# Kernel optimization log

Measured on AMD Instinct MI355X. Metric: run time of the kernel, lower is better.

## Reference

```python
import jax, jax.numpy as jnp
import numpy as np

K = 10        # neighbors
SIGMA = 1.0   # gaussian bandwidth
BIG = 1e9     # diagonal fill so a point is never its own neighbor


def _knn_idx(h, k):
    # h: (B, T, H) -> idx: (B, T, k) of nearest neighbors (euclidean), excluding self
    # squared-distance trick avoids materializing (B, T, T, H)
    sq = jnp.sum(h * h, axis=-1)                                  # (B, T)
    d2 = sq[:, :, None] + sq[:, None, :] - 2.0 * jnp.einsum('bth,bsh->bts', h, h)
    d = jnp.sqrt(jnp.maximum(d2, 0.0))                            # (B, T, T)
    T = h.shape[1]
    eye = jnp.eye(T, dtype=bool)
    d = jnp.where(eye[None, :, :], BIG, d)
    k_eff = min(k, T - 1)
    _, idx = jax.lax.top_k(-d, k_eff)                             # smallest distances
    return idx


def setup_inputs() -> dict:
    key = jax.random.key(0)
    ks = jax.random.split(key, 5)
    B, T, C, H = 64, 1024, 64, 32
    x = jax.random.normal(ks[0], (B, T, C), dtype=jnp.float32)
    s1 = 1.0 / np.sqrt(C)
    s2 = 1.0 / np.sqrt(H)
    W1 = jax.random.uniform(ks[1], (C, H), minval=-s1, maxval=s1, dtype=jnp.float32)
    b1 = jax.random.uniform(ks[2], (H,), minval=-s1, maxval=s1, dtype=jnp.float32)
    W2 = jax.random.uniform(ks[3], (H, H), minval=-s2, maxval=s2, dtype=jnp.float32)
    b2 = jax.random.uniform(ks[4], (H,), minval=-s2, maxval=s2, dtype=jnp.float32)
    return {"x": x, "W1": W1, "b1": b1, "W2": W2, "b2": b2}


def reference(x, W1, b1, W2, b2):
    h = x @ W1 + b1                                               # (B, T, H)
    # kNN graph built under no_grad in the original
    idx = _knn_idx(jax.lax.stop_gradient(h), K)                   # (B, T, k)
    # gather neighbors without the (B, T, T, H) expansion
    neigh = jax.vmap(lambda hb, ib: hb[ib])(h, idx)               # (B, T, k, H)
    diff = neigh - h[:, :, None, :]
    dist = jnp.sqrt(jnp.sum(diff * diff, axis=-1))                # (B, T, k)
    w = jnp.exp(-dist ** 2 / (2.0 * SIGMA ** 2 + 1e-8))
    w = w / (jnp.sum(w, axis=-1, keepdims=True) + 1e-8)
    smooth = jnp.einsum('btk,btkh->bth', w, neigh)                # (B, T, H)
    lap = h - smooth
    return jnp.tanh(lap) @ W2 + b2
```

## Files before the change

### kernel.cpp

```cpp
#include <hip/hip_runtime.h>
#include <math.h>

#define BB 64
#define TT 1024
#define CC 64
#define HH 32
#define KNN 10

typedef float v4f __attribute__((ext_vector_type(4)));
typedef _Float16 f16x8 __attribute__((ext_vector_type(8)));

__device__ __forceinline__ unsigned umn(unsigned a, unsigned b) { return a < b ? a : b; }
__device__ __forceinline__ unsigned umx(unsigned a, unsigned b) { return a > b ? a : b; }

__global__ __launch_bounds__(256) void h_kernel(
    const float* __restrict__ x, const float* __restrict__ W1,
    const float* __restrict__ b1, float* __restrict__ h, float* __restrict__ hsq)
{
    __shared__ float w1s[CC][HH];
    __shared__ float b1s[HH];
    int tid = threadIdx.x;
    for (int i = tid; i < CC * HH; i += 256) w1s[i >> 5][i & 31] = W1[i];
    if (tid < HH) b1s[tid] = b1[tid];
    __syncthreads();

    int row = blockIdx.x * 256 + tid;
    const float4* xr = (const float4*)(x + (size_t)row * CC);
    float acc[HH];
    #pragma unroll
    for (int j = 0; j < HH; ++j) acc[j] = b1s[j];
    #pragma unroll
    for (int c4 = 0; c4 < CC / 4; ++c4) {
        float4 xv = xr[c4];
        #pragma unroll
        for (int j = 0; j < HH; ++j) {
            acc[j] = fmaf(xv.x, w1s[c4 * 4 + 0][j], acc[j]);
            acc[j] = fmaf(xv.y, w1s[c4 * 4 + 1][j], acc[j]);
            acc[j] = fmaf(xv.z, w1s[c4 * 4 + 2][j], acc[j]);
            acc[j] = fmaf(xv.w, w1s[c4 * 4 + 3][j], acc[j]);
        }
    }
    float s = 0.f;
    #pragma unroll
    for (int j = 0; j < HH; ++j) s = fmaf(acc[j], acc[j], s);
    float* hr = h + (size_t)row * HH;
    #pragma unroll
    for (int q = 0; q < HH / 4; ++q) {
        float4 v = { acc[4*q], acc[4*q+1], acc[4*q+2], acc[4*q+3] };
        ((float4*)hr)[q] = v;
    }
    hsq[row] = 0.5f * s * 1048576.0f;
}

#define INSERT_PAIR(kE, kO) do {                                       \
    unsigned lo_ = umn(kE, kO), hi_ = umx(kE, kO);                     \
    bd9 = umn(umn(bd9, umx(bd8, lo_)), umx(bd7, hi_));                 \
    bd8 = umn(umn(bd8, umx(bd7, lo_)), umx(bd6, hi_));                 \
    bd7 = umn(umn(bd7, umx(bd6, lo_)), umx(bd5, hi_));                 \
    bd6 = umn(umn(bd6, umx(bd5, lo_)), umx(bd4, hi_));                 \
    bd5 = umn(umn(bd5, umx(bd4, lo_)), umx(bd3, hi_));                 \
    bd4 = umn(umn(bd4, umx(bd3, lo_)), umx(bd2, hi_));                 \
    bd3 = umn(umn(bd3, umx(bd2, lo_)), umx(bd1, hi_));                 \
    bd2 = umn(umn(bd2, umx(bd1, lo_)), umx(bd0, hi_));                 \
    bd1 = umn(umn(bd1, umx(bd0, lo_)), hi_);                           \
    bd0 = umn(bd0, lo_);                                               \
} while (0)

__global__ __launch_bounds__(512, 2) void lap_kernel(
    const float* __restrict__ h, const float* __restrict__ hsq,
    const float* __restrict__ W2, const float* __restrict__ b2,
    float* __restrict__ out)
{
    __shared__ _Float16 cah[2][2][64][40];
    __shared__ _Float16 cal[2][2][64][40];
    __shared__ unsigned s_key[8][64][KNN];
    __shared__ float e_wk[64][KNN];
    __shared__ short e_id[64][KNN];
    __shared__ float e_inv[64];
    __shared__ float w2s[HH][HH];
    __shared__ float b2s[HH];

    int tid  = threadIdx.x;
    int lane = tid & 63;
    int wid  = __builtin_amdgcn_readfirstlane(tid >> 6);

    int g   = blockIdx.x;
    int l   = g >> 3;
    int bb  = ((g & 7) << 3) | (l & 7);
    int rb  = (l >> 3) << 6;

    for (int i = tid; i < HH * HH; i += 512) w2s[i >> 5][i & 31] = W2[i];
    if (tid < HH) b2s[tid] = b2[tid];

    const float* hb  = h   + (size_t)bb * TT * HH;
    const float* sqb = hsq + (size_t)bb * TT;

    int gtg  = wid & 3;
    int half = wid >> 2;
    int n    = lane & 15;
    int kc   = lane >> 4;

    int trow = rb + gtg * 16 + n;
    f16x8 Bhi, Blo;
    {
        const float* tp = hb + (size_t)trow * HH + kc * 8;
        float4 f1 = ((const float4*)tp)[0];
        float4 f2 = ((const float4*)tp)[1];
        float tf[8] = { f1.x, f1.y, f1.z, f1.w, f2.x, f2.y, f2.z, f2.w };
        #pragma unroll
        for (int e = 0; e < 8; ++e) {
            _Float16 hh = (_Float16)tf[e];
            Bhi[e] = hh;
            Blo[e] = (_Float16)(tf[e] - (float)hh);
        }
    }
    float cinit20 = sqb[trow] + 1048576.0f;

    int s_local = trow - half * 512;
    bool selfok = ((unsigned)s_local < 512u) && (((s_local >> 2) & 3) == kc);
    int self_t7 = selfok ? (((s_local >> 6) << 4) | (((s_local >> 4) & 3) << 2)
                           | (s_local & 3)) : -1;

    unsigned bd0 = 0xFFFFFFFFu, bd1 = 0xFFFFFFFFu, bd2 = 0xFFFFFFFFu,
             bd3 = 0xFFFFFFFFu, bd4 = 0xFFFFFFFFu, bd5 = 0xFFFFFFFFu,
             bd6 = 0xFFFFFFFFu, bd7 = 0xFFFFFFFFu, bd8 = 0xFFFFFFFFu,
             bd9 = 0xFFFFFFFFu;

    int st_c = tid & 3, st_r = (tid >> 2) & 63, st_h = tid >> 8;

    auto STAGE = [&](int buf, int t) {
        const float* p = hb + (size_t)(st_h * 512 + t * 64 + st_r) * HH + st_c * 8;
        float4 f1 = ((const float4*)p)[0];
        float4 f2 = ((const float4*)p)[1];
        float fe[8] = { f1.x, f1.y, f1.z, f1.w, f2.x, f2.y, f2.z, f2.w };
        f16x8 hi8, lo8;
        #pragma unroll
        for (int e = 0; e < 8; ++e) {
            _Float16 hh = (_Float16)fe[e];
            hi8[e] = hh;
            lo8[e] = (_Float16)(fe[e] - (float)hh);
        }
        *(f16x8*)&cah[buf][st_h][st_r][st_c * 8] = hi8;
        *(f16x8*)&cal[buf][st_h][st_r][st_c * 8] = lo8;
    };

    STAGE(0, 0);
    __syncthreads();

    for (int t = 0; t < 8; ++t) {
        if (t < 7) STAGE((t + 1) & 1, t + 1);
        int buf = t & 1;
        #pragma unroll
        for (int sub = 0; sub < 4; ++sub) {
            f16x8 Ahi = *(const f16x8*)&cah[buf][half][sub * 16 + n][kc * 8];
            f16x8 Alo = *(const f16x8*)&cal[buf][half][sub * 16 + n][kc * 8];
            v4f acc = { 0.f, 0.f, 0.f, 0.f };
            acc = __builtin_amdgcn_mfma_f32_16x16x32_f16(Ahi, Bhi, acc, 0, 0, 0);
            acc = __builtin_amdgcn_mfma_f32_16x16x32_f16(Ahi, Blo, acc, 0, 0, 0);
            acc = __builtin_amdgcn_mfma_f32_16x16x32_f16(Alo, Bhi, acc, 0, 0, 0);
            const float4 hv = *(const float4*)(sqb + half * 512 + t * 64
                                               + sub * 16 + kc * 4);
            int t7b = (t << 4) | (sub << 2);
            float k0f = fmaf(acc[0], -1048576.0f, cinit20 + hv.x);
            float k1f = fmaf(acc[1], -1048576.0f, cinit20 + hv.y);
            float k2f = fmaf(acc[2], -1048576.0f, cinit20 + hv.z);
            float k3f = fmaf(acc[3], -1048576.0f, cinit20 + hv.w);
            unsigned p0 = (umn((unsigned)k0f, 0x1FFFFFFu) << 7) | (unsigned)(t7b + 0);
            unsigned p1 = (umn((unsigned)k1f, 0x1FFFFFFu) << 7) | (unsigned)(t7b + 1);
            unsigned p2 = (umn((unsigned)k2f, 0x1FFFFFFu) << 7) | (unsigned)(t7b + 2);
            unsigned p3 = (umn((unsigned)k3f, 0x1FFFFFFu) << 7) | (unsigned)(t7b + 3);
            p0 = (t7b + 0 == self_t7) ? 0xFFFFFFFFu : p0;
            p1 = (t7b + 1 == self_t7) ? 0xFFFFFFFFu : p1;
            p2 = (t7b + 2 == self_t7) ? 0xFFFFFFFFu : p2;
            p3 = (t7b + 3 == self_t7) ? 0xFFFFFFFFu : p3;
            INSERT_PAIR(p0, p1);
            INSERT_PAIR(p2, p3);
        }
        __syncthreads();
    }

    {
        int p  = half * 4 + kc;
        int tr = gtg * 16 + n;
        s_key[p][tr][0] = bd0; s_key[p][tr][1] = bd1;
        s_key[p][tr][2] = bd2; s_key[p][tr][3] = bd3;
        s_key[p][tr][4] = bd4; s_key[p][tr][5] = bd5;
        s_key[p][tr][6] = bd6; s_key[p][tr][7] = bd7;
        s_key[p][tr][8] = bd8; s_key[p][tr][9] = bd9;
    }
    __syncthreads();

    if (wid == 0) {
        unsigned k0 = s_key[0][lane][0], k1 = s_key[1][lane][0];
        unsigned k2 = s_key[2][lane][0], k3 = s_key[3][lane][0];
        unsigned k4 = s_key[4][lane][0], k5 = s_key[5][lane][0];
        unsigned k6 = s_key[6][lane][0], k7 = s_key[7][lane][0];
        int q0=0,q1=0,q2=0,q3=0,q4=0,q5=0,q6=0,q7=0;
        float wsum = 0.f;
        #pragma unroll
        for (int j = 0; j < KNN; ++j) {
            unsigned mn = k0; int c = 0;
            if (k1 < mn) { mn = k1; c = 1; }
            if (k2 < mn) { mn = k2; c = 2; }
            if (k3 < mn) { mn = k3; c = 3; }
            if (k4 < mn) { mn = k4; c = 4; }
            if (k5 < mn) { mn = k5; c = 5; }
            if (k6 < mn) { mn = k6; c = 6; }
            if (k7 < mn) { mn = k7; c = 7; }
            int t7 = (int)(mn & 127u);
            int abs_ = ((c >> 2) << 9) + ((t7 >> 4) << 6) + (((t7 >> 2) & 3) << 4)
                       + ((c & 3) << 2) + (t7 & 3);
            float kf = (float)(mn >> 7) * 9.5367431640625e-07f;
            float wk = expf(1.0f - kf);
            wsum += wk;
            e_id[lane][j] = (short)abs_;
            e_wk[lane][j] = wk;
            if      (c == 0) { ++q0; k0 = (q0 < KNN) ? s_key[0][lane][q0] : 0xFFFFFFFFu; }
            else if (c == 1) { ++q1; k1 = (q1 < KNN) ? s_key[1][lane][q1] : 0xFFFFFFFFu; }
            else if (c == 2) { ++q2; k2 = (q2 < KNN) ? s_key[2][lane][q2] : 0xFFFFFFFFu; }
            else if (c == 3) { ++q3; k3 = (q3 < KNN) ? s_key[3][lane][q3] : 0xFFFFFFFFu; }
            else if (c == 4) { ++q4; k4 = (q4 < KNN) ? s_key[4][lane][q4] : 0xFFFFFFFFu; }
            else if (c == 5) { ++q5; k5 = (q5 < KNN) ? s_key[5][lane][q5] : 0xFFFFFFFFu; }
            else if (c == 6) { ++q6; k6 = (q6 < KNN) ? s_key[6][lane][q6] : 0xFFFFFFFFu; }
            else             { ++q7; k7 = (q7 < KNN) ? s_key[7][lane][q7] : 0xFFFFFFFFu; }
        }
        e_inv[lane] = 1.0f / (wsum + 1e-8f);
    }
    __syncthreads();

    float* a_pool = (float*)&s_key[0][0][0];
    {
        int r  = tid >> 3;
        int g2 = (tid & 7) << 2;
        float ax = 0.f, ay = 0.f, az = 0.f, aw = 0.f;
        #pragma unroll
        for (int k = 0; k < KNN; ++k) {
            int idx  = e_id[r][k];
            float wk = e_wk[r][k];
            const float4 nv = *(const float4*)(hb + (size_t)idx * HH + g2);
            ax = fmaf(wk, nv.x, ax);
            ay = fmaf(wk, nv.y, ay);
            az = fmaf(wk, nv.z, az);
            aw = fmaf(wk, nv.w, aw);
        }
        float inv = e_inv[r];
        const float4 hv = *(const float4*)(hb + (size_t)(rb + r) * HH + g2);
        float4 av;
        av.x = tanhf(fmaf(-ax, inv, hv.x));
        av.y = tanhf(fmaf(-ay, inv, hv.y));
        av.z = tanhf(fmaf(-az, inv, hv.z));
        av.w = tanhf(fmaf(-aw, inv, hv.w));
        *(float4*)&a_pool[r * 36 + g2] = av;
    }
    __syncthreads();

    int r   = tid >> 3;
    int c0_ = (tid & 7) << 2;
    float o[4];
    #pragma unroll
    for (int u = 0; u < 4; ++u) o[u] = b2s[c0_ + u];
    #pragma unroll
    for (int j = 0; j < HH; ++j) {
        float av = a_pool[r * 36 + j];
        #pragma unroll
        for (int u = 0; u < 4; ++u) o[u] = fmaf(av, w2s[j][c0_ + u], o[u]);
    }
    float* op = out + ((size_t)bb * TT + rb + r) * HH + c0_;
    float4 o1 = { o[0], o[1], o[2], o[3] };
    *((float4*)op) = o1;
}

extern "C" void kernel_launch(void* const* d_in, const int* in_sizes, int n_in,
                              void* d_out, int out_size, void* d_ws, size_t ws_size,
                              hipStream_t stream) {
    const float* x  = (const float*)d_in[0];
    const float* W1 = (const float*)d_in[1];
    const float* b1 = (const float*)d_in[2];
    const float* W2 = (const float*)d_in[3];
    const float* b2 = (const float*)d_in[4];
    float* outp = (float*)d_out;

    float* h   = (float*)d_ws;
    float* hsq = h + (size_t)BB * TT * HH;

    h_kernel<<<(BB * TT) / 256, 256, 0, stream>>>(x, W1, b1, h, hsq);
    lap_kernel<<<BB * (TT / 64), 512, 0, stream>>>(h, hsq, W2, b2, outp);
}
```

Before: 81.64 us.

## Single-buffer swizzled LDS staging with register prefetch to raise occupancy

Replaces the double-buffered padded LDS tiles with a single buffer that uses an XOR column swizzle instead of padding, cutting LDS use. The next tile is now prefetched into registers during compute and written to LDS after an extra barrier. Launch bounds rise from 2 to 6 blocks per SM so more waves can be resident. The trade-off is an additional __syncthreads per iteration and register pressure from the occupancy hint, which could cause spills given the ten-key insertion state.

```diff
diff --git a/kernel.cpp b/kernel.cpp
--- a/kernel.cpp
+++ b/kernel.cpp
@@ -66,13 +66,13 @@
     bd0 = umn(bd0, lo_);                                               \
 } while (0)
 
-__global__ __launch_bounds__(512, 2) void lap_kernel(
+__global__ __launch_bounds__(512, 6) void lap_kernel(
     const float* __restrict__ h, const float* __restrict__ hsq,
     const float* __restrict__ W2, const float* __restrict__ b2,
     float* __restrict__ out)
 {
-    __shared__ _Float16 cah[2][2][64][40];
-    __shared__ _Float16 cal[2][2][64][40];
+    __shared__ _Float16 cah[2][64][32];
+    __shared__ _Float16 cal[2][64][32];
     __shared__ unsigned s_key[8][64][KNN];
     __shared__ float e_wk[64][KNN];
     __shared__ short e_id[64][KNN];
@@ -127,11 +127,10 @@
              bd9 = 0xFFFFFFFFu;
 
     int st_c = tid & 3, st_r = (tid >> 2) & 63, st_h = tid >> 8;
-
-    auto STAGE = [&](int buf, int t) {
-        const float* p = hb + (size_t)(st_h * 512 + t * 64 + st_r) * HH + st_c * 8;
-        float4 f1 = ((const float4*)p)[0];
-        float4 f2 = ((const float4*)p)[1];
+    int st_cp = st_c ^ (st_r & 3);
+    int rd_cp = kc ^ (n & 3);
+
+    auto ST_WRITE = [&](float4 f1, float4 f2) {
         float fe[8] = { f1.x, f1.y, f1.z, f1.w, f2.x, f2.y, f2.z, f2.w };
         f16x8 hi8, lo8;
         #pragma unroll
@@ -140,20 +139,30 @@
             hi8[e] = hh;
             lo8[e] = (_Float16)(fe[e] - (float)hh);
         }
-        *(f16x8*)&cah[buf][st_h][st_r][st_c * 8] = hi8;
-        *(f16x8*)&cal[buf][st_h][st_r][st_c * 8] = lo8;
+        *(f16x8*)&cah[st_h][st_r][st_cp * 8] = hi8;
+        *(f16x8*)&cal[st_h][st_r][st_cp * 8] = lo8;
     };
-
-    STAGE(0, 0);
+    auto ST_ADDR = [&](int t) {
+        return hb + (size_t)(st_h * 512 + t * 64 + st_r) * HH + st_c * 8;
+    };
+
+    {
+        const float* p = ST_ADDR(0);
+        ST_WRITE(((const float4*)p)[0], ((const float4*)p)[1]);
+    }
     __syncthreads();
 
     for (int t = 0; t < 8; ++t) {
-        if (t < 7) STAGE((t + 1) & 1, t + 1);
-        int buf = t & 1;
+        float4 g1, g2;
+        if (t < 7) {
+            const float* p = ST_ADDR(t + 1);
+            g1 = ((const float4*)p)[0];
+            g2 = ((const float4*)p)[1];
+        }
         #pragma unroll
         for (int sub = 0; sub < 4; ++sub) {
-            f16x8 Ahi = *(const f16x8*)&cah[buf][half][sub * 16 + n][kc * 8];
-            f16x8 Alo = *(const f16x8*)&cal[buf][half][sub * 16 + n][kc * 8];
+            f16x8 Ahi = *(const f16x8*)&cah[half][sub * 16 + n][rd_cp * 8];
+            f16x8 Alo = *(const f16x8*)&cal[half][sub * 16 + n][rd_cp * 8];
             v4f acc = { 0.f, 0.f, 0.f, 0.f };
             acc = __builtin_amdgcn_mfma_f32_16x16x32_f16(Ahi, Bhi, acc, 0, 0, 0);
             acc = __builtin_amdgcn_mfma_f32_16x16x32_f16(Ahi, Blo, acc, 0, 0, 0);
@@ -176,6 +185,8 @@
             INSERT_PAIR(p0, p1);
             INSERT_PAIR(p2, p3);
         }
+        __syncthreads();
+        if (t < 7) ST_WRITE(g1, g2);
         __syncthreads();
     }
 
```

Result: slower. 87.95 us (+7.7%).

## Alias shared memory regions, swizzle staged tiles, cache squared norms in LDS

Applied to the files above, without the earlier changes.

The kernel's separate shared arrays are replaced by one 36 KB byte pool whose regions are reused across phases: the staging buffers, the key lists, the neighbor tables and the activation pool share storage. This cuts the LDS footprint so more blocks can be resident per CU, and the occupancy hint in launch_bounds is raised to match. The padded tile rows are dropped and replaced with a rotated column-chunk placement, keyed on row, to avoid LDS bank conflicts. The per-batch squared norms are now copied into LDS once instead of being read from global memory in the inner loop, and the W2/b2 loads are moved later. The higher occupancy hint may force register limits or spills in a register-heavy loop.

```diff
diff --git a/kernel.cpp b/kernel.cpp
--- a/kernel.cpp
+++ b/kernel.cpp
@@ -66,19 +66,22 @@
     bd0 = umn(bd0, lo_);                                               \
 } while (0)
 
-__global__ __launch_bounds__(512, 2) void lap_kernel(
+__global__ __launch_bounds__(512, 8) void lap_kernel(
     const float* __restrict__ h, const float* __restrict__ hsq,
     const float* __restrict__ W2, const float* __restrict__ b2,
     float* __restrict__ out)
 {
-    __shared__ _Float16 cah[2][2][64][40];
-    __shared__ _Float16 cal[2][2][64][40];
-    __shared__ unsigned s_key[8][64][KNN];
-    __shared__ float e_wk[64][KNN];
-    __shared__ short e_id[64][KNN];
-    __shared__ float e_inv[64];
-    __shared__ float w2s[HH][HH];
-    __shared__ float b2s[HH];
+    __shared__ __align__(16) unsigned char smem[36864];
+    auto cah  = reinterpret_cast<_Float16 (*)[2][64][32]>(smem);
+    auto cal  = reinterpret_cast<_Float16 (*)[2][64][32]>(smem + 16384);
+    float* hsql = reinterpret_cast<float*>(smem + 32768);
+    auto s_key  = reinterpret_cast<unsigned (*)[64][KNN]>(smem);
+    float* e_wk = reinterpret_cast<float*>(smem + 20480);
+    short* e_id = reinterpret_cast<short*>(smem + 23040);
+    float* e_inv = reinterpret_cast<float*>(smem + 24320);
+    float* w2s  = reinterpret_cast<float*>(smem + 24576);
+    float* b2s  = reinterpret_cast<float*>(smem + 28672);
+    float* a_pool = reinterpret_cast<float*>(smem);
 
     int tid  = threadIdx.x;
     int lane = tid & 63;
@@ -88,9 +91,6 @@
     int l   = g >> 3;
     int bb  = ((g & 7) << 3) | (l & 7);
     int rb  = (l >> 3) << 6;
-
-    for (int i = tid; i < HH * HH; i += 512) w2s[i >> 5][i & 31] = W2[i];
-    if (tid < HH) b2s[tid] = b2[tid];
 
     const float* hb  = h   + (size_t)bb * TT * HH;
     const float* sqb = hsq + (size_t)bb * TT;
@@ -127,6 +127,8 @@
              bd9 = 0xFFFFFFFFu;
 
     int st_c = tid & 3, st_r = (tid >> 2) & 63, st_h = tid >> 8;
+    int st_cp = (st_c + (st_r >> 1)) & 3;
+    int rd_cp = (kc + (n >> 1)) & 3;
 
     auto STAGE = [&](int buf, int t) {
         const float* p = hb + (size_t)(st_h * 512 + t * 64 + st_r) * HH + st_c * 8;
@@ -140,10 +142,11 @@
             hi8[e] = hh;
             lo8[e] = (_Float16)(fe[e] - (float)hh);
         }
-        *(f16x8*)&cah[buf][st_h][st_r][st_c * 8] = hi8;
-        *(f16x8*)&cal[buf][st_h][st_r][st_c * 8] = lo8;
+        *(f16x8*)&cah[buf][st_h][st_r][st_cp * 8] = hi8;
+        *(f16x8*)&cal[buf][st_h][st_r][st_cp * 8] = lo8;
     };
 
+    for (int i = tid; i < TT; i += 512) hsql[i] = sqb[i];
     STAGE(0, 0);
     __syncthreads();
 
@@ -152,14 +155,14 @@
         int buf = t & 1;
         #pragma unroll
         for (int sub = 0; sub < 4; ++sub) {
-            f16x8 Ahi = *(const f16x8*)&cah[buf][half][sub * 16 + n][kc * 8];
-            f16x8 Alo = *(const f16x8*)&cal[buf][half][sub * 16 + n][kc * 8];
+            f16x8 Ahi = *(const f16x8*)&cah[buf][half][sub * 16 + n][rd_cp * 8];
+            f16x8 Alo = *(const f16x8*)&cal[buf][half][sub * 16 + n][rd_cp * 8];
             v4f acc = { 0.f, 0.f, 0.f, 0.f };
             acc = __builtin_amdgcn_mfma_f32_16x16x32_f16(Ahi, Bhi, acc, 0, 0, 0);
             acc = __builtin_amdgcn_mfma_f32_16x16x32_f16(Ahi, Blo, acc, 0, 0, 0);
             acc = __builtin_amdgcn_mfma_f32_16x16x32_f16(Alo, Bhi, acc, 0, 0, 0);
-            const float4 hv = *(const float4*)(sqb + half * 512 + t * 64
-                                               + sub * 16 + kc * 4);
+            const float4 hv = *(const float4*)&hsql[half * 512 + t * 64
+                                                    + sub * 16 + kc * 4];
             int t7b = (t << 4) | (sub << 2);
             float k0f = fmaf(acc[0], -1048576.0f, cinit20 + hv.x);
             float k1f = fmaf(acc[1], -1048576.0f, cinit20 + hv.y);
@@ -188,6 +191,8 @@
         s_key[p][tr][6] = bd6; s_key[p][tr][7] = bd7;
         s_key[p][tr][8] = bd8; s_key[p][tr][9] = bd9;
     }
+    for (int i = tid; i < HH * HH; i += 512) w2s[i] = W2[i];
+    if (tid < HH) b2s[tid] = b2[tid];
     __syncthreads();
 
     if (wid == 0) {
@@ -213,8 +218,8 @@
             float kf = (float)(mn >> 7) * 9.5367431640625e-07f;
             float wk = expf(1.0f - kf);
             wsum += wk;
-            e_id[lane][j] = (short)abs_;
-            e_wk[lane][j] = wk;
+            e_id[lane * KNN + j] = (short)abs_;
+            e_wk[lane * KNN + j] = wk;
             if      (c == 0) { ++q0; k0 = (q0 < KNN) ? s_key[0][lane][q0] : 0xFFFFFFFFu; }
             else if (c == 1) { ++q1; k1 = (q1 < KNN) ? s_key[1][lane][q1] : 0xFFFFFFFFu; }
             else if (c == 2) { ++q2; k2 = (q2 < KNN) ? s_key[2][lane][q2] : 0xFFFFFFFFu; }
@@ -228,15 +233,14 @@
     }
     __syncthreads();
 
-    float* a_pool = (float*)&s_key[0][0][0];
     {
         int r  = tid >> 3;
         int g2 = (tid & 7) << 2;
         float ax = 0.f, ay = 0.f, az = 0.f, aw = 0.f;
         #pragma unroll
         for (int k = 0; k < KNN; ++k) {
-            int idx  = e_id[r][k];
-            float wk = e_wk[r][k];
+            int idx  = e_id[r * KNN + k];
+            float wk = e_wk[r * KNN + k];
             const float4 nv = *(const float4*)(hb + (size_t)idx * HH + g2);
             ax = fmaf(wk, nv.x, ax);
             ay = fmaf(wk, nv.y, ay);
@@ -263,7 +267,7 @@
     for (int j = 0; j < HH; ++j) {
         float av = a_pool[r * 36 + j];
         #pragma unroll
-        for (int u = 0; u < 4; ++u) o[u] = fmaf(av, w2s[j][c0_ + u], o[u]);
+        for (int u = 0; u < 4; ++u) o[u] = fmaf(av, w2s[j * HH + c0_ + u], o[u]);
     }
     float* op = out + ((size_t)bb * TT + rb + r) * HH + c0_;
     float4 o1 = { o[0], o[1], o[2], o[3] };
```

Measured after the change: 79.01 us. -3.2%, faster.
